# Kernel optimization log

Measured on AMD Instinct MI355X. Metric: run time of the kernel, lower is better.

## Reference

```python
import jax, jax.numpy as jnp
import numpy as np

B, T, D, H = 4, 2048, 1024, 16
DEPTH = D // H
MASK_NEG = 1e10


def setup_inputs() -> dict:
    key = jax.random.key(0)
    k1, k2, k3 = jax.random.split(key, 3)
    x = jax.random.normal(k1, (B, T, D), dtype=jnp.float32)
    w_attn = jax.random.normal(k2, (D, 3 * D), dtype=jnp.float32) * 0.02
    b_attn = jnp.zeros((3 * D,), dtype=jnp.float32)
    w_proj = jax.random.normal(k3, (D, D), dtype=jnp.float32) * 0.02
    b_proj = jnp.zeros((D,), dtype=jnp.float32)
    return {"x": x, "w_attn": w_attn, "b_attn": b_attn,
            "w_proj": w_proj, "b_proj": b_proj}


def _split_heads(t):
    # (B, T, D) -> (B, H, T, depth)
    return t.reshape(B, T, H, DEPTH).transpose(0, 2, 1, 3)


def reference(x, w_attn, b_attn, w_proj, b_proj):
    # fused QKV projection (GPT-2 conv1d == dense)
    qkv = x @ w_attn + b_attn                      # (B, T, 3D)
    q, k, v = jnp.split(qkv, 3, axis=2)
    q, k, v = _split_heads(q), _split_heads(k), _split_heads(v)
    present = jnp.stack([k, v], axis=1)            # (B, 2, H, T, depth)

    # scaled scores with additive causal mask (as in source: w*b - 1e10*(1-b))
    scores = jnp.einsum('bhqd,bhkd->bhqk', q, k) / jnp.sqrt(
        jnp.asarray(DEPTH, dtype=x.dtype))
    i = jnp.arange(T)[:, None]
    j = jnp.arange(T)[None, :]
    b = (i >= j).astype(scores.dtype)              # (T, T) lower-tri incl diag
    scores = scores * b - MASK_NEG * (1.0 - b)
    attn = jax.nn.softmax(scores, axis=-1)         # (B, H, T, T)

    out = jnp.einsum('bhqk,bhkd->bhqd', attn, v)   # (B, H, T, depth)
    out = out.transpose(0, 2, 1, 3).reshape(B, T, D)
    out = out @ w_proj + b_proj                    # (B, T, D)
    return out, present
```

## Files before the change

kernel.cpp:

```cpp
#include <hip/hip_runtime.h>
#include <hip/hip_bf16.h>
#include <cstdint>
#include <cstddef>

typedef __bf16 y8 __attribute__((ext_vector_type(8)));
typedef float f4 __attribute__((ext_vector_type(4)));
typedef unsigned short u16t;

#define NB 4
#define TT 2048
#define DD 1024
#define HH 16

static constexpr size_t OUT0 = (size_t)NB * TT * DD;
#define QSCALE 0.180336880111120426f

__device__ __forceinline__ u16t bf16r(float f) {
    union { float f; unsigned u; } x; x.f = f;
    return (u16t)((x.u + 0x7FFFu + ((x.u >> 16) & 1u)) >> 16);
}

__device__ __forceinline__ unsigned cvtpk(float lo, float hi) {
    unsigned r;
    asm("v_cvt_pk_bf16_f32 %0, %1, %2" : "=v"(r) : "v"(lo), "v"(hi));
    return r;
}

#define GLDS16(g, s) __builtin_amdgcn_global_load_lds( \
    (__attribute__((address_space(1))) void*)(g),      \
    (__attribute__((address_space(3))) void*)(s), 16, 0, 0)

#define BARX() asm volatile("s_barrier" ::: "memory")
#define VMW(n) asm volatile("s_waitcnt vmcnt(" #n ")" ::: "memory")
#define LGKM0() asm volatile("s_waitcnt lgkmcnt(0)" ::: "memory")

__global__ __launch_bounds__(256)
void prep(const float* __restrict__ x, u16t* __restrict__ xb,
          const float* __restrict__ w_attn, u16t* __restrict__ wta,
          const float* __restrict__ w_proj, u16t* __restrict__ wtp)
{
    const int bid = blockIdx.x;
    if (bid < 4096) {
        const int i = (bid * 256 + threadIdx.x) * 8;
        float4 a = *(const float4*)(x + i);
        float4 b = *(const float4*)(x + i + 4);
        union { u16t h[8]; uint4 q; } u;
        u.h[0] = bf16r(a.x); u.h[1] = bf16r(a.y); u.h[2] = bf16r(a.z); u.h[3] = bf16r(a.w);
        u.h[4] = bf16r(b.x); u.h[5] = bf16r(b.y); u.h[6] = bf16r(b.z); u.h[7] = bf16r(b.w);
        *(uint4*)(xb + i) = u.q;
        return;
    }
    __shared__ float tile[32][33];
    const float* in; u16t* outp; int Nd, n0, k0, qlim; float qs;
    if (bid < 7168) {
        const int j = bid - 4096;
        in = w_attn; outp = wta; Nd = 3072;
        n0 = (j % 96) * 32; k0 = (j / 96) * 32; qlim = 1024; qs = QSCALE;
    } else {
        const int j = bid - 7168;
        in = w_proj; outp = wtp; Nd = 1024;
        n0 = (j & 31) * 32; k0 = (j >> 5) * 32; qlim = 0; qs = 1.0f;
    }
    const int tx = threadIdx.x & 31, ty = threadIdx.x >> 5;
    for (int yy = ty; yy < 32; yy += 8)
        tile[yy][tx] = in[(size_t)(k0 + yy) * Nd + n0 + tx];
    __syncthreads();
    for (int yy = ty; yy < 32; yy += 8) {
        float v = tile[tx][yy];
        if (n0 + yy < qlim) v *= qs;
        outp[(size_t)(n0 + yy) * 1024 + k0 + tx] = bf16r(v);
    }
}

template<int MODE>
__global__ __launch_bounds__(512, 1)
void gemm_bt(const u16t* __restrict__ A, const u16t* __restrict__ Bt,
             const float* __restrict__ bias, float* __restrict__ C,
             float* __restrict__ pres, u16t* __restrict__ qb,
             u16t* __restrict__ kb, u16t* __restrict__ vtb,
             int N, int K)
{
    __shared__ char sm[98304];
    char* const smA0 = sm;
    char* const smB0 = sm + 65536;
    const int tid = threadIdx.x;
    const int w = tid >> 6, l = tid & 63;
    const int wr = w >> 1, wc = w & 1;
    const int lr = l & 15, lq = l >> 4;
    const int idx = blockIdx.x;
    const int bm = (idx & 31) << 8;
    const int bn = (idx >> 5) << 7;

    auto stage = [&](int k0, int pi) {
#pragma unroll
        for (int c = 0; c < 4; ++c) {
            const int L = (tid << 4) + (c << 13);
            const int row = L >> 7;
            const int col = (((L >> 4) & 7) ^ (row & 7)) << 3;
            GLDS16(A + (size_t)(bm + row) * K + k0 + col,
                   smA0 + (pi << 15) + L);
        }
#pragma unroll
        for (int c = 0; c < 2; ++c) {
            const int L = (tid << 4) + (c << 13);
            const int row = L >> 7;
            const int col = (((L >> 4) & 7) ^ (row & 7)) << 3;
            GLDS16(Bt + (size_t)(bn + row) * K + k0 + col,
                   smB0 + (pi << 14) + L);
        }
    };

    f4 acc[4][4] = {};
    const int nt = K >> 6;

    stage(0, 0);
    for (int t = 0; t < nt; ++t) {
        if (t + 1 < nt) { stage((t + 1) << 6, (t + 1) & 1); VMW(6); }
        else            { VMW(0); }
        BARX();
        const char* La = smA0 + ((t & 1) << 15);
        const char* Lb = smB0 + ((t & 1) << 14);
#pragma unroll
        for (int ks = 0; ks < 2; ++ks) {
            y8 af[4], bfv[4];
#pragma unroll
            for (int m = 0; m < 4; ++m) {
                const int row = wr * 64 + m * 16 + lr;
                const int slot = (lq + ks * 4) ^ (row & 7);
                af[m] = *(const y8*)(La + row * 128 + (slot << 4));
            }
#pragma unroll
            for (int n = 0; n < 4; ++n) {
                const int row = wc * 64 + n * 16 + lr;
                const int slot = (lq + ks * 4) ^ (row & 7);
                bfv[n] = *(const y8*)(Lb + row * 128 + (slot << 4));
            }
#pragma unroll
            for (int m = 0; m < 4; ++m)
#pragma unroll
                for (int n = 0; n < 4; ++n)
                    acc[m][n] = __builtin_amdgcn_mfma_f32_16x16x32_bf16(af[m], bfv[n], acc[m][n], 0, 0, 0);
        }
        BARX();
    }

    if (MODE == 0) {
#pragma unroll
        for (int m = 0; m < 4; ++m) {
            const int rowb = bm + wr * 64 + m * 16 + 4 * lq;
#pragma unroll
            for (int n = 0; n < 4; ++n) {
                const int col = bn + wc * 64 + n * 16 + lr;
                const float bv = bias[col];
#pragma unroll
                for (int r = 0; r < 4; ++r)
                    C[(size_t)(rowb + r) * N + col] = acc[m][n][r] + bv;
            }
        }
    } else {
        const int part = bn >> 10;

        if (part == 2) {
#pragma unroll
            for (int m = 0; m < 4; ++m) {
                const int rowb = bm + wr * 64 + m * 16 + 4 * lq;
                const int b0 = rowb >> 11, t0 = rowb & 2047;
#pragma unroll
                for (int n = 0; n < 4; ++n) {
                    const int colg = bn + wc * 64 + n * 16 + lr;
                    const float bv = bias[colg];
                    const int cl = colg & 1023;
                    const int h = cl >> 6, d = cl & 63;
                    uint2 pk;
                    pk.x = cvtpk(acc[m][n][0] + bv, acc[m][n][1] + bv);
                    pk.y = cvtpk(acc[m][n][2] + bv, acc[m][n][3] + bv);
                    *(uint2*)(vtb + ((size_t)(b0 * HH + h) * 64 + d) * TT + t0) = pk;
                }
            }
        }

#pragma unroll
        for (int m = 0; m < 4; ++m)
#pragma unroll
            for (int n = 0; n < 4; ++n) {
                const int co = wc * 64 + n * 16 + lr;
                float bv = bias[bn + co];
                if (part == 0) bv *= QSCALE;
#pragma unroll
                for (int r = 0; r < 4; ++r) {
                    const int ro = wr * 64 + m * 16 + 4 * lq + r;
                    *(u16t*)(smA0 + ro * 256 + (((co >> 3) ^ (ro & 7)) << 4)
                             + ((co & 7) << 1)) = bf16r(acc[m][n][r] + bv);
                }
            }
        LGKM0();
        BARX();

        const int hb = (bn & 1023) >> 6;
        const int c = tid & 15;
        const int rw = tid >> 4;
        const int h2 = hb + (c >> 3);
        const int d0 = (c & 7) * 8;
#pragma unroll
        for (int s = 0; s < 8; ++s) {
            const int row = s * 32 + rw;
            union { y8 v; uint4 q; u16t h[8]; } u;
            u.v = *(const y8*)(smA0 + row * 256 + ((c ^ (row & 7)) << 4));
            const int tglob = bm + row;
            const int b0 = tglob >> 11, tt = tglob & 2047;
            const size_t base = (((size_t)(b0 * HH + h2)) * TT + tt) * 64 + d0;
            if (part == 0) {
                *(uint4*)(qb + base) = u.q;
            } else {
                if (part == 1) *(uint4*)(kb + base) = u.q;
                float4 f0, f1;
                f0.x = __uint_as_float((unsigned)u.h[0] << 16);
                f0.y = __uint_as_float((unsigned)u.h[1] << 16);
                f0.z = __uint_as_float((unsigned)u.h[2] << 16);
                f0.w = __uint_as_float((unsigned)u.h[3] << 16);
                f1.x = __uint_as_float((unsigned)u.h[4] << 16);
                f1.y = __uint_as_float((unsigned)u.h[5] << 16);
                f1.z = __uint_as_float((unsigned)u.h[6] << 16);
                f1.w = __uint_as_float((unsigned)u.h[7] << 16);
                const size_t pb = OUT0 +
                    (((size_t)((b0 * 2 + (part - 1)) * HH + h2)) * TT + tt) * 64 + d0;
                *(float4*)(pres + pb) = f0;
                *(float4*)(pres + pb + 4) = f1;
            }
        }
    }
}

__global__ __launch_bounds__(256, 3)
void attn_fwd(const u16t* __restrict__ qg, const u16t* __restrict__ kg,
              const u16t* __restrict__ vtg, u16t* __restrict__ og)
{
    __shared__ u16t sQP[128 * 64];
    __shared__ u16t sK[2 * 64 * 64];
    __shared__ u16t sV[2 * 64 * 64];
    const int tid = threadIdx.x;
    const int w = tid >> 6, l = tid & 63;
    const int lr = l & 15, lq = l >> 4;
    const int qt = 15 - blockIdx.y;
    const int bh = blockIdx.x;
    const int b = bh >> 4, h = bh & 15;
    const u16t* qsrc = qg + (size_t)bh * TT * 64;
    const u16t* ksrc = kg + (size_t)bh * TT * 64;
    const u16t* vsrc = vtg + (size_t)bh * 64 * TT;

    auto stageKV = [&](int kt, int pi) {
        const int kv0 = kt << 6;
#pragma unroll
        for (int c = 0; c < 2; ++c) {
            const int L = ((w * 64 + l) << 4) + (c << 12);
            const int row = L >> 7;
            const int col = (((L >> 4) & 7) ^ (row & 7)) << 3;
            GLDS16(ksrc + (kv0 + row) * 64 + col,
                   (char*)sK + (pi << 13) + (w << 10) + (c << 12));
            GLDS16(vsrc + (size_t)row * TT + kv0 + col,
                   (char*)sV + (pi << 13) + (w << 10) + (c << 12));
        }
    };

#pragma unroll
    for (int c = 0; c < 4; ++c) {
        const int L = ((w * 64 + l) << 4) + (c << 12);
        const int row = L >> 7;
        const int col = (((L >> 4) & 7) ^ (row & 7)) << 3;
        GLDS16(qsrc + (qt * 128 + row) * 64 + col, (char*)sQP + (w << 10) + (c << 12));
    }
    stageKV(0, 0);
    __syncthreads();

    y8 qf[2][2];
#pragma unroll
    for (int qm = 0; qm < 2; ++qm)
#pragma unroll
        for (int ks = 0; ks < 2; ++ks) {
            const int row = w * 32 + qm * 16 + lr;
            const int slot = (lq + ks * 4) ^ (row & 7);
            qf[qm][ks] = *(const y8*)((const char*)sQP + row * 128 + (slot << 4));
        }

    f4 o[2][4] = {};
    float lsum[2] = {0.f, 0.f};

    char* Pw = (char*)sQP + (w << 12);
    const int qmax = qt * 128 + w * 32 + 31;
    const int ktiles = 2 * qt + 2;
    int cur = 0;

    for (int kt = 0; kt < ktiles; ++kt) {
        __syncthreads();
        if (kt + 1 < ktiles) stageKV(kt + 1, cur ^ 1);
        const int kv0 = kt << 6;
        if (kv0 <= qmax) {
            const char* Kb = (const char*)sK + (cur << 13);
            const char* Vb = (const char*)sV + (cur << 13);

            f4 s[2][4] = {};
            __builtin_amdgcn_s_setprio(1);
#pragma unroll
            for (int ks = 0; ks < 2; ++ks) {
                y8 kf[4];
#pragma unroll
                for (int n = 0; n < 4; ++n) {
                    const int row = n * 16 + lr;
                    const int slot = (lq + ks * 4) ^ (row & 7);
                    kf[n] = *(const y8*)(Kb + row * 128 + (slot << 4));
                }
#pragma unroll
                for (int qm = 0; qm < 2; ++qm)
#pragma unroll
                    for (int n = 0; n < 4; ++n)
                        s[qm][n] = __builtin_amdgcn_mfma_f32_16x16x32_bf16(kf[n], qf[qm][ks], s[qm][n], 0, 0, 0);
            }
            __builtin_amdgcn_s_setprio(0);

#pragma unroll
            for (int qm = 0; qm < 2; ++qm) {
                const int qb0 = qt * 128 + w * 32 + qm * 16;
                if (kv0 + 63 > qb0) {
                    const int query = qb0 + lr;
#pragma unroll
                    for (int n = 0; n < 4; ++n)
#pragma unroll
                        for (int r = 0; r < 4; ++r)
                            if (kv0 + n * 16 + 4 * lq + r > query) s[qm][n][r] = -1e30f;
                }

                float rs = 0.f;
#pragma unroll
                for (int n = 0; n < 4; ++n)
#pragma unroll
                    for (int r = 0; r < 4; ++r) {
                        const float p = exp2f(s[qm][n][r]);
                        s[qm][n][r] = p;
                        rs += p;
                    }
                lsum[qm] += rs;

                const int prow = qm * 16 + lr;
                const int rbase = prow * 128 + ((lq & 1) << 3);
#pragma unroll
                for (int n = 0; n < 4; ++n) {
                    uint2 pk;
                    pk.x = cvtpk(s[qm][n][0], s[qm][n][1]);
                    pk.y = cvtpk(s[qm][n][2], s[qm][n][3]);
                    const int sIdx = 2 * n + (lq >> 1);
                    *(uint2*)(Pw + rbase + ((sIdx ^ (prow & 7)) << 4)) = pk;
                }
            }

            __builtin_amdgcn_s_setprio(1);
#pragma unroll
            for (int ks = 0; ks < 2; ++ks) {
                y8 vf[4], pf[2];
#pragma unroll
                for (int n = 0; n < 4; ++n) {
                    const int row = n * 16 + lr;
                    const int slot = (lq + ks * 4) ^ (row & 7);
                    vf[n] = *(const y8*)(Vb + row * 128 + (slot << 4));
                }
#pragma unroll
                for (int qm = 0; qm < 2; ++qm) {
                    const int row = qm * 16 + lr;
                    const int slot = (lq + ks * 4) ^ (row & 7);
                    pf[qm] = *(const y8*)(Pw + row * 128 + (slot << 4));
                }
#pragma unroll
                for (int qm = 0; qm < 2; ++qm)
#pragma unroll
                    for (int n = 0; n < 4; ++n)
                        o[qm][n] = __builtin_amdgcn_mfma_f32_16x16x32_bf16(vf[n], pf[qm], o[qm][n], 0, 0, 0);
            }
            __builtin_amdgcn_s_setprio(0);
        }
        cur ^= 1;
    }

#pragma unroll
    for (int qm = 0; qm < 2; ++qm) {
        float t = lsum[qm];
        t += __shfl_xor(t, 16);
        t += __shfl_xor(t, 32);
        const float inv = 1.0f / t;
        const int trow = qt * 128 + w * 32 + qm * 16 + lr;
#pragma unroll
        for (int n = 0; n < 4; ++n) {
            uint2 pk;
            pk.x = cvtpk(o[qm][n][0] * inv, o[qm][n][1] * inv);
            pk.y = cvtpk(o[qm][n][2] * inv, o[qm][n][3] * inv);
            *(uint2*)(og + ((size_t)(b * TT + trow)) * DD + h * 64 + n * 16 + 4 * lq) = pk;
        }
    }
}

extern "C" void kernel_launch(void* const* d_in, const int* in_sizes, int n_in,
                              void* d_out, int out_size, void* d_ws, size_t ws_size,
                              hipStream_t stream) {
    const float* x      = (const float*)d_in[0];
    const float* w_attn = (const float*)d_in[1];
    const float* b_attn = (const float*)d_in[2];
    const float* w_proj = (const float*)d_in[3];
    const float* b_proj = (const float*)d_in[4];
    float* outp = (float*)d_out;
    char* ws = (char*)d_ws;

    u16t* xb  = (u16t*)(ws + 0);
    u16t* wta = (u16t*)(ws + 16777216);
    u16t* wtp = (u16t*)(ws + 23068672);
    u16t* qb  = (u16t*)(ws + 25165824);
    u16t* kb  = (u16t*)(ws + 41943040);
    u16t* vtb = (u16t*)(ws + 58720256);
    if (ws_size < 75497472) return;

    prep<<<8192, 256, 0, stream>>>(x, xb, w_attn, wta, w_proj, wtp);

    gemm_bt<1><<<768, 512, 0, stream>>>(xb, wta, b_attn, nullptr, outp,
                                        qb, kb, vtb, 3072, 1024);
    attn_fwd<<<dim3(64, 16), 256, 0, stream>>>(qb, kb, vtb, xb );
    gemm_bt<0><<<256, 512, 0, stream>>>(xb, wtp, b_proj, outp,
                                        nullptr, nullptr, nullptr, nullptr,
                                        1024, 1024);
}
```

Measured before the change: 165.3 us.

## Split QKV GEMM into 256x256-tile Q/K kernel and separate V kernel

The fused QKV projection GEMM is split in two. A new kernel computes the Q and K columns with 256x256 output tiles, giving more data reuse per staged byte. The existing kernel, given a column offset, now handles only the V columns and writes V transposed plus its present slice. This trades one extra kernel launch and 128KB of shared memory per block (lower occupancy, more accumulator registers) for higher arithmetic intensity and less branching in the epilogue.

```diff
diff --git a/kernel.cpp b/kernel.cpp
--- a/kernel.cpp
+++ b/kernel.cpp
@@ -72,13 +72,124 @@
     }
 }
 
+__global__ __launch_bounds__(512, 1)
+void gemm_qk(const u16t* __restrict__ A, const u16t* __restrict__ Bt,
+             const float* __restrict__ bias, float* __restrict__ pres,
+             u16t* __restrict__ qb, u16t* __restrict__ kb)
+{
+    constexpr int K = 1024;
+    __shared__ char sm[131072];
+    char* const smA0 = sm;
+    char* const smB0 = sm + 65536;
+    const int tid = threadIdx.x;
+    const int w = tid >> 6, l = tid & 63;
+    const int wr = w >> 1, wc = w & 1;
+    const int lr = l & 15, lq = l >> 4;
+    const int bm = (blockIdx.x & 31) << 8;
+    const int bn = (blockIdx.x >> 5) << 8;
+
+    auto stage = [&](int k0, int pi) {
+#pragma unroll
+        for (int c = 0; c < 4; ++c) {
+            const int L = (tid << 4) + (c << 13);
+            const int row = L >> 7;
+            const int col = (((L >> 4) & 7) ^ (row & 7)) << 3;
+            GLDS16(A + (size_t)(bm + row) * K + k0 + col, smA0 + (pi << 15) + L);
+            GLDS16(Bt + (size_t)(bn + row) * K + k0 + col, smB0 + (pi << 15) + L);
+        }
+    };
+
+    f4 acc[4][8] = {};
+    const int nt = K >> 6;
+
+    stage(0, 0);
+    for (int t = 0; t < nt; ++t) {
+        if (t + 1 < nt) { stage((t + 1) << 6, (t + 1) & 1); VMW(8); }
+        else            { VMW(0); }
+        BARX();
+        const char* La = smA0 + ((t & 1) << 15);
+        const char* Lb = smB0 + ((t & 1) << 15);
+#pragma unroll
+        for (int ks = 0; ks < 2; ++ks) {
+            y8 af[4], bfv[8];
+#pragma unroll
+            for (int m = 0; m < 4; ++m) {
+                const int row = wr * 64 + m * 16 + lr;
+                const int slot = (lq + ks * 4) ^ (row & 7);
+                af[m] = *(const y8*)(La + row * 128 + (slot << 4));
+            }
+#pragma unroll
+            for (int n = 0; n < 8; ++n) {
+                const int row = wc * 128 + n * 16 + lr;
+                const int slot = (lq + ks * 4) ^ (row & 7);
+                bfv[n] = *(const y8*)(Lb + row * 128 + (slot << 4));
+            }
+#pragma unroll
+            for (int m = 0; m < 4; ++m)
+#pragma unroll
+                for (int n = 0; n < 8; ++n)
+                    acc[m][n] = __builtin_amdgcn_mfma_f32_16x16x32_bf16(af[m], bfv[n], acc[m][n], 0, 0, 0);
+        }
+        BARX();
+    }
+
+    const int part = bn >> 10;
+
+#pragma unroll
+    for (int m = 0; m < 4; ++m)
+#pragma unroll
+        for (int n = 0; n < 8; ++n) {
+            const int co = wc * 128 + n * 16 + lr;
+            float bv = bias[bn + co];
+            if (part == 0) bv *= QSCALE;
+#pragma unroll
+            for (int r = 0; r < 4; ++r) {
+                const int ro = wr * 64 + m * 16 + 4 * lq + r;
+                *(u16t*)(sm + ro * 512 + ((((co >> 3) ^ (ro & 7))) << 4)
+                         + ((co & 7) << 1)) = bf16r(acc[m][n][r] + bv);
+            }
+        }
+    LGKM0();
+    BARX();
+
+    const int c = tid & 31;
+    const int rw = tid >> 5;
+    const int h2 = ((bn & 1023) >> 6) + (c >> 3);
+    const int d0 = (c & 7) * 8;
+#pragma unroll
+    for (int s = 0; s < 16; ++s) {
+        const int row = s * 16 + rw;
+        union { y8 v; uint4 q; u16t h[8]; } u;
+        u.v = *(const y8*)(sm + row * 512 + ((c ^ (row & 7)) << 4));
+        const int tglob = bm + row;
+        const int b0 = tglob >> 11, tt = tglob & 2047;
+        const size_t base = (((size_t)(b0 * HH + h2)) * TT + tt) * 64 + d0;
+        if (part == 0) {
+            *(uint4*)(qb + base) = u.q;
+        } else {
+            *(uint4*)(kb + base) = u.q;
+            float4 f0, f1;
+            f0.x = __uint_as_float((unsigned)u.h[0] << 16);
+            f0.y = __uint_as_float((unsigned)u.h[1] << 16);
+            f0.z = __uint_as_float((unsigned)u.h[2] << 16);
+            f0.w = __uint_as_float((unsigned)u.h[3] << 16);
+            f1.x = __uint_as_float((unsigned)u.h[4] << 16);
+            f1.y = __uint_as_float((unsigned)u.h[5] << 16);
+            f1.z = __uint_as_float((unsigned)u.h[6] << 16);
+            f1.w = __uint_as_float((unsigned)u.h[7] << 16);
+            const size_t pb = OUT0 + (((size_t)(b0 * 2 * HH + h2)) * TT + tt) * 64 + d0;
+            *(float4*)(pres + pb) = f0;
+            *(float4*)(pres + pb + 4) = f1;
+        }
+    }
+}
+
 template<int MODE>
 __global__ __launch_bounds__(512, 1)
 void gemm_bt(const u16t* __restrict__ A, const u16t* __restrict__ Bt,
              const float* __restrict__ bias, float* __restrict__ C,
-             float* __restrict__ pres, u16t* __restrict__ qb,
-             u16t* __restrict__ kb, u16t* __restrict__ vtb,
-             int N, int K)
+             float* __restrict__ pres, u16t* __restrict__ vtb,
+             int N, int K, int bnoff)
 {
     __shared__ char sm[98304];
     char* const smA0 = sm;
@@ -89,7 +200,7 @@
     const int lr = l & 15, lq = l >> 4;
     const int idx = blockIdx.x;
     const int bm = (idx & 31) << 8;
-    const int bn = (idx >> 5) << 7;
+    const int bn = bnoff + ((idx >> 5) << 7);
 
     auto stage = [&](int k0, int pi) {
 #pragma unroll
@@ -97,16 +208,14 @@
             const int L = (tid << 4) + (c << 13);
             const int row = L >> 7;
             const int col = (((L >> 4) & 7) ^ (row & 7)) << 3;
-            GLDS16(A + (size_t)(bm + row) * K + k0 + col,
-                   smA0 + (pi << 15) + L);
+            GLDS16(A + (size_t)(bm + row) * K + k0 + col, smA0 + (pi << 15) + L);
         }
 #pragma unroll
         for (int c = 0; c < 2; ++c) {
             const int L = (tid << 4) + (c << 13);
             const int row = L >> 7;
             const int col = (((L >> 4) & 7) ^ (row & 7)) << 3;
-            GLDS16(Bt + (size_t)(bn + row) * K + k0 + col,
-                   smB0 + (pi << 14) + L);
+            GLDS16(Bt + (size_t)(bn + row) * K + k0 + col, smB0 + (pi << 14) + L);
         }
     };
 
@@ -158,24 +267,20 @@
             }
         }
     } else {
-        const int part = bn >> 10;
-
-        if (part == 2) {
-#pragma unroll
-            for (int m = 0; m < 4; ++m) {
-                const int rowb = bm + wr * 64 + m * 16 + 4 * lq;
-                const int b0 = rowb >> 11, t0 = rowb & 2047;
-#pragma unroll
-                for (int n = 0; n < 4; ++n) {
-                    const int colg = bn + wc * 64 + n * 16 + lr;
-                    const float bv = bias[colg];
-                    const int cl = colg & 1023;
-                    const int h = cl >> 6, d = cl & 63;
-                    uint2 pk;
-                    pk.x = cvtpk(acc[m][n][0] + bv, acc[m][n][1] + bv);
-                    pk.y = cvtpk(acc[m][n][2] + bv, acc[m][n][3] + bv);
-                    *(uint2*)(vtb + ((size_t)(b0 * HH + h) * 64 + d) * TT + t0) = pk;
-                }
+#pragma unroll
+        for (int m = 0; m < 4; ++m) {
+            const int rowb = bm + wr * 64 + m * 16 + 4 * lq;
+            const int b0 = rowb >> 11, t0 = rowb & 2047;
+#pragma unroll
+            for (int n = 0; n < 4; ++n) {
+                const int colg = bn + wc * 64 + n * 16 + lr;
+                const float bv = bias[colg];
+                const int cl = colg & 1023;
+                const int h = cl >> 6, d = cl & 63;
+                uint2 pk;
+                pk.x = cvtpk(acc[m][n][0] + bv, acc[m][n][1] + bv);
+                pk.y = cvtpk(acc[m][n][2] + bv, acc[m][n][3] + bv);
+                *(uint2*)(vtb + ((size_t)(b0 * HH + h) * 64 + d) * TT + t0) = pk;
             }
         }
 
@@ -184,8 +289,7 @@
 #pragma unroll
             for (int n = 0; n < 4; ++n) {
                 const int co = wc * 64 + n * 16 + lr;
-                float bv = bias[bn + co];
-                if (part == 0) bv *= QSCALE;
+                const float bv = bias[bn + co];
 #pragma unroll
                 for (int r = 0; r < 4; ++r) {
                     const int ro = wr * 64 + m * 16 + 4 * lq + r;
@@ -208,25 +312,19 @@
             u.v = *(const y8*)(smA0 + row * 256 + ((c ^ (row & 7)) << 4));
             const int tglob = bm + row;
             const int b0 = tglob >> 11, tt = tglob & 2047;
-            const size_t base = (((size_t)(b0 * HH + h2)) * TT + tt) * 64 + d0;
-            if (part == 0) {
-                *(uint4*)(qb + base) = u.q;
-            } else {
-                if (part == 1) *(uint4*)(kb + base) = u.q;
-                float4 f0, f1;
-                f0.x = __uint_as_float((unsigned)u.h[0] << 16);
-                f0.y = __uint_as_float((unsigned)u.h[1] << 16);
-                f0.z = __uint_as_float((unsigned)u.h[2] << 16);
-                f0.w = __uint_as_float((unsigned)u.h[3] << 16);
-                f1.x = __uint_as_float((unsigned)u.h[4] << 16);
-                f1.y = __uint_as_float((unsigned)u.h[5] << 16);
-                f1.z = __uint_as_float((unsigned)u.h[6] << 16);
-                f1.w = __uint_as_float((unsigned)u.h[7] << 16);
-                const size_t pb = OUT0 +
-                    (((size_t)((b0 * 2 + (part - 1)) * HH + h2)) * TT + tt) * 64 + d0;
-                *(float4*)(pres + pb) = f0;
-                *(float4*)(pres + pb + 4) = f1;
-            }
+            float4 f0, f1;
+            f0.x = __uint_as_float((unsigned)u.h[0] << 16);
+            f0.y = __uint_as_float((unsigned)u.h[1] << 16);
+            f0.z = __uint_as_float((unsigned)u.h[2] << 16);
+            f0.w = __uint_as_float((unsigned)u.h[3] << 16);
+            f1.x = __uint_as_float((unsigned)u.h[4] << 16);
+            f1.y = __uint_as_float((unsigned)u.h[5] << 16);
+            f1.z = __uint_as_float((unsigned)u.h[6] << 16);
+            f1.w = __uint_as_float((unsigned)u.h[7] << 16);
+            const size_t pb = OUT0 +
+                (((size_t)((b0 * 2 + 1) * HH + h2)) * TT + tt) * 64 + d0;
+            *(float4*)(pres + pb) = f0;
+            *(float4*)(pres + pb + 4) = f1;
         }
     }
 }
@@ -417,10 +515,10 @@
 
     prep<<<8192, 256, 0, stream>>>(x, xb, w_attn, wta, w_proj, wtp);
 
-    gemm_bt<1><<<768, 512, 0, stream>>>(xb, wta, b_attn, nullptr, outp,
-                                        qb, kb, vtb, 3072, 1024);
+    gemm_qk<<<256, 512, 0, stream>>>(xb, wta, b_attn, outp, qb, kb);
+    gemm_bt<1><<<256, 512, 0, stream>>>(xb, wta, b_attn, nullptr, outp, vtb,
+                                        3072, 1024, 2048);
     attn_fwd<<<dim3(64, 16), 256, 0, stream>>>(qb, kb, vtb, xb );
-    gemm_bt<0><<<256, 512, 0, stream>>>(xb, wtp, b_proj, outp,
-                                        nullptr, nullptr, nullptr, nullptr,
-                                        1024, 1024);
-}
+    gemm_bt<0><<<256, 512, 0, stream>>>(xb, wtp, b_proj, outp, nullptr, nullptr,
+                                        1024, 1024, 0);
+}
```

After: 166.6 us. About the same (+0.8%).
